# Kernel optimization log

Hardware: AMD Instinct MI355X
Metric: run time of the kernel (lower is better)

Reference implementation:

```python
import jax, jax.numpy as jnp
import numpy as np

NUM_NODES = 100000
IN_CH = 128
OUT_CH = 64
NUM_EDGES = 1000000


def setup_inputs() -> dict:
    key = jax.random.key(0)
    ks = jax.random.split(key, 16)

    x = jax.random.normal(ks[0], (NUM_NODES, IN_CH), dtype=jnp.float32)

    def make_edges(k_src, k_tgt, k_w):
        src = jax.random.randint(k_src, (NUM_EDGES,), 0, NUM_NODES, dtype=jnp.int32)
        # tf.math.segment_sum requires sorted segment ids -> sort targets
        tgt = jnp.sort(jax.random.randint(k_tgt, (NUM_EDGES,), 0, NUM_NODES, dtype=jnp.int32))
        ei = jnp.stack([src, tgt], axis=0)  # (2, E)
        ew = jax.random.uniform(k_w, (NUM_EDGES,), dtype=jnp.float32)
        return ei, ew

    edge_index_in, edge_weight_in = make_edges(ks[1], ks[2], ks[3])
    edge_index_out, edge_weight_out = make_edges(ks[4], ks[5], ks[6])

    glorot = (6.0 / (IN_CH + OUT_CH)) ** 0.5
    W_main_in = jax.random.uniform(ks[7], (IN_CH, OUT_CH), minval=-glorot, maxval=glorot, dtype=jnp.float32)
    W_main_out = jax.random.uniform(ks[8], (IN_CH, OUT_CH), minval=-glorot, maxval=glorot, dtype=jnp.float32)
    W_shared = jax.random.uniform(ks[9], (IN_CH, OUT_CH), minval=-glorot, maxval=glorot, dtype=jnp.float32)

    bias_main_in = jnp.zeros((OUT_CH,), dtype=jnp.float32)
    bias_main_out = jnp.zeros((OUT_CH,), dtype=jnp.float32)
    bias_shared_in = jnp.zeros((OUT_CH,), dtype=jnp.float32)
    bias_shared_out = jnp.zeros((OUT_CH,), dtype=jnp.float32)

    C_in_vec = jnp.ones((NUM_NODES, 1), dtype=jnp.float32)
    C_out_vec = jnp.ones((NUM_NODES, 1), dtype=jnp.float32)

    return {
        "x": x,
        "W_main_in": W_main_in,
        "W_main_out": W_main_out,
        "W_shared": W_shared,
        "bias_main_in": bias_main_in,
        "bias_main_out": bias_main_out,
        "bias_shared_in": bias_shared_in,
        "bias_shared_out": bias_shared_out,
        "C_in_vec": C_in_vec,
        "C_out_vec": C_out_vec,
        "edge_index_in": edge_index_in,
        "edge_weight_in": edge_weight_in,
        "edge_index_out": edge_index_out,
        "edge_weight_out": edge_weight_out,
    }


def _propagate(h, edge_index, edge_weight, num_nodes):
    # gather messages from source nodes, scale by edge weight, sum into targets
    src = edge_index[0]
    tgt = edge_index[1]
    msgs = h[src] * edge_weight[:, None]  # (E, OUT_CH)
    return jax.ops.segment_sum(msgs, tgt, num_segments=num_nodes)  # (N, OUT_CH)


def reference(x, W_main_in, W_main_out, W_shared,
              bias_main_in, bias_main_out, bias_shared_in, bias_shared_out,
              C_in_vec, C_out_vec,
              edge_index_in, edge_weight_in, edge_index_out, edge_weight_out):
    n = x.shape[0]
    h_main_in = _propagate(x @ W_main_in, edge_index_in, edge_weight_in, n)
    h_shared_in = _propagate(x @ W_shared, edge_index_in, edge_weight_in, n)
    ic_combined = h_main_in + bias_main_in + (h_shared_in + bias_shared_in)

    h_main_out = _propagate(x @ W_main_out, edge_index_out, edge_weight_out, n)
    h_shared_out = _propagate(x @ W_shared, edge_index_out, edge_weight_out, n)
    oc_combined = h_main_out + bias_main_out + (h_shared_out + bias_shared_out)

    return C_in_vec * ic_combined + C_out_vec * oc_combined
```

## Files before the change

### kernel.cpp

```cpp
#include <hip/hip_runtime.h>

#define IN_CH   128
#define OUT_CH  64
#define M_TILE  128
#define XS_PITCH 136

typedef __attribute__((ext_vector_type(8))) short short8;
typedef __attribute__((ext_vector_type(4))) float floatx4;

__device__ __forceinline__ unsigned short f2bf(float f) {
    union { float f; unsigned u; } v; v.f = f;
    unsigned r = v.u + 0x7fffu + ((v.u >> 16) & 1u);
    return (unsigned short)(r >> 16);
}
__device__ __forceinline__ float bf2f(unsigned v) {
    union { unsigned u; float f; } c; c.u = v << 16;
    return c.f;
}

__global__ void prep_kernel(const int* __restrict__ tgtIn,
                            const int* __restrict__ tgtOut,
                            const float* __restrict__ Wmi,
                            const float* __restrict__ Wmo,
                            const float* __restrict__ Wsh,
                            int* __restrict__ rpIn,
                            int* __restrict__ rpOut,
                            unsigned short* __restrict__ WcT,
                            int n_nodes, int neIn, int neOut)
{
    int i = blockIdx.x * blockDim.x + threadIdx.x;
    int half = n_nodes + 1;
    if (i < 2 * half) {
        const int* tgt; int* rp; int t; int ne;
        if (i < half) { tgt = tgtIn;  rp = rpIn;  t = i;        ne = neIn; }
        else          { tgt = tgtOut; rp = rpOut; t = i - half; ne = neOut; }
        int lo = 0, hi = ne;
        while (lo < hi) {
            int mid = (lo + hi) >> 1;
            if (tgt[mid] < t) lo = mid + 1; else hi = mid;
        }
        rp[t] = lo;
    } else {
        int j = i - 2 * half;
        if (j < 2 * OUT_CH * IN_CH) {
            int n = j >> 7, k = j & 127;
            float m = (n < OUT_CH) ? Wmi[k * OUT_CH + n]
                                   : Wmo[k * OUT_CH + (n - OUT_CH)];
            float s = Wsh[k * OUT_CH + (n & (OUT_CH - 1))];
            WcT[n * IN_CH + k] = f2bf(m + s);
        }
    }
}

__global__ __launch_bounds__(256, 3)
void gemm_kernel(const float* __restrict__ x,
                 const unsigned short* __restrict__ WcT,
                 unsigned short* __restrict__ Abf,
                 unsigned short* __restrict__ Bbf,
                 int n_nodes)
{
    __shared__ unsigned short Xs[M_TILE][XS_PITCH];

    const int tid  = threadIdx.x;
    const int w    = tid >> 6;
    const int lane = tid & 63;
    const int l15  = lane & 15;
    const int quad = lane >> 4;
    const long long node0 = (long long)blockIdx.x * M_TILE;

    short8 bfrag[4][2];
#pragma unroll
    for (int ks = 0; ks < 4; ++ks)
#pragma unroll
        for (int ni = 0; ni < 2; ++ni)
            bfrag[ks][ni] = *(const short8*)&WcT[(w * 32 + ni * 16 + l15) * IN_CH
                                                 + ks * 32 + quad * 8];

    {
        const float4* x4 = (const float4*)x;
        for (int i = tid; i < M_TILE * (IN_CH / 4); i += 256) {
            int row = i >> 5, c4 = i & 31;
            long long node = node0 + row;
            float4 v = make_float4(0.f, 0.f, 0.f, 0.f);
            if (node < n_nodes) v = x4[node * (IN_CH / 4) + c4];
            uint2 p;
            p.x = ((unsigned)f2bf(v.y) << 16) | f2bf(v.x);
            p.y = ((unsigned)f2bf(v.w) << 16) | f2bf(v.z);
            *(uint2*)&Xs[row][c4 * 4] = p;
        }
    }
    __syncthreads();

    floatx4 acc[8][2];
#pragma unroll
    for (int mi = 0; mi < 8; ++mi)
#pragma unroll
        for (int ni = 0; ni < 2; ++ni)
            acc[mi][ni] = (floatx4){0.f, 0.f, 0.f, 0.f};

#pragma unroll
    for (int ks = 0; ks < 4; ++ks) {
        const int k0 = ks * 32 + quad * 8;
#pragma unroll
        for (int mi = 0; mi < 8; ++mi) {
            short8 a = *(const short8*)&Xs[mi * 16 + l15][k0];
            acc[mi][0] = __builtin_amdgcn_mfma_f32_16x16x32_bf16(a, bfrag[ks][0], acc[mi][0], 0, 0, 0);
            acc[mi][1] = __builtin_amdgcn_mfma_f32_16x16x32_bf16(a, bfrag[ks][1], acc[mi][1], 0, 0, 0);
        }
    }

    unsigned short* Hout = (w < 2) ? Abf : Bbf;
    const int colb = (w & 1) * 32;
#pragma unroll
    for (int mi = 0; mi < 8; ++mi)
#pragma unroll
        for (int ni = 0; ni < 2; ++ni)
#pragma unroll
            for (int r = 0; r < 4; ++r) {
                long long row = node0 + mi * 16 + quad * 4 + r;
                if (row < n_nodes)
                    Hout[row * OUT_CH + colb + ni * 16 + l15] = f2bf(acc[mi][ni][r]);
            }
}

__device__ __forceinline__
float segsum(const unsigned short* __restrict__ Hl, int e0, int e1,
             const int* __restrict__ src, const float* __restrict__ ew,
             int lane)
{
    float a0 = 0.f, a1 = 0.f, a2 = 0.f, a3 = 0.f;
    for (int base = e0; base < e1; base += 64) {
        int cnt = min(64, e1 - base);
        int s = 0; float w = 0.f;
        if (lane < cnt) { s = src[base + lane]; w = ew[base + lane]; }
        for (int j = 0; j < cnt; j += 8) {
            int sj[8]; float wj[8];
#pragma unroll
            for (int i = 0; i < 8; ++i) {
                int idx = j + i;
                int sel = (idx < cnt) ? idx : 0;
                sj[i] = __builtin_amdgcn_readlane(s, sel);
                int wi = __builtin_amdgcn_readlane(__float_as_int(w), sel);
                wj[i] = (idx < cnt) ? __int_as_float(wi) : 0.f;
            }
            float v[8];
#pragma unroll
            for (int i = 0; i < 8; ++i)
                v[i] = bf2f(Hl[(long long)sj[i] * OUT_CH]);
            a0 += wj[0] * v[0]; a1 += wj[1] * v[1];
            a2 += wj[2] * v[2]; a3 += wj[3] * v[3];
            a0 += wj[4] * v[4]; a1 += wj[5] * v[5];
            a2 += wj[6] * v[6]; a3 += wj[7] * v[7];
        }
    }
    return (a0 + a1) + (a2 + a3);
}

__global__ __launch_bounds__(256)
void prop_kernel(const unsigned short* __restrict__ A,
                 const unsigned short* __restrict__ B,
                 const int* __restrict__ rpIn, const int* __restrict__ rpOut,
                 const int* __restrict__ srcIn, const float* __restrict__ ewIn,
                 const int* __restrict__ srcOut, const float* __restrict__ ewOut,
                 const float* __restrict__ bmi, const float* __restrict__ bmo,
                 const float* __restrict__ bsi, const float* __restrict__ bso,
                 const float* __restrict__ Cin, const float* __restrict__ Cout,
                 float* __restrict__ out, int n_nodes)
{
    const int lane = threadIdx.x & 63;
    const int wv = __builtin_amdgcn_readfirstlane(threadIdx.x >> 6);
    const int t = blockIdx.x * 4 + wv;
    if (t >= n_nodes) return;

    float bin  = bmi[lane] + bsi[lane];
    float bout = bmo[lane] + bso[lane];
    float ci = Cin[t], co = Cout[t];

    int ei0 = __builtin_amdgcn_readfirstlane(rpIn[t]);
    int ei1 = __builtin_amdgcn_readfirstlane(rpIn[t + 1]);
    int eo0 = __builtin_amdgcn_readfirstlane(rpOut[t]);
    int eo1 = __builtin_amdgcn_readfirstlane(rpOut[t + 1]);

    float ic = segsum(A + lane, ei0, ei1, srcIn, ewIn, lane);
    float oc = segsum(B + lane, eo0, eo1, srcOut, ewOut, lane);

    out[t * OUT_CH + lane] = ci * (ic + bin) + co * (oc + bout);
}

extern "C" void kernel_launch(void* const* d_in, const int* in_sizes, int n_in,
                              void* d_out, int out_size, void* d_ws, size_t ws_size,
                              hipStream_t stream)
{
    const float* x    = (const float*)d_in[0];
    const float* Wmi  = (const float*)d_in[1];
    const float* Wmo  = (const float*)d_in[2];
    const float* Wsh  = (const float*)d_in[3];
    const float* bmi  = (const float*)d_in[4];
    const float* bmo  = (const float*)d_in[5];
    const float* bsi  = (const float*)d_in[6];
    const float* bso  = (const float*)d_in[7];
    const float* Cin  = (const float*)d_in[8];
    const float* Cout = (const float*)d_in[9];
    const int*   eiIn  = (const int*)d_in[10];
    const float* ewIn  = (const float*)d_in[11];
    const int*   eiOut = (const int*)d_in[12];
    const float* ewOut = (const float*)d_in[13];

    const int n_nodes = in_sizes[0] / IN_CH;
    const int neIn  = in_sizes[11];
    const int neOut = in_sizes[13];

    const int* srcIn  = eiIn;
    const int* tgtIn  = eiIn + neIn;
    const int* srcOut = eiOut;
    const int* tgtOut = eiOut + neOut;

    char* ws = (char*)d_ws;
    size_t NH = (size_t)n_nodes * OUT_CH * sizeof(unsigned short);
    unsigned short* Abf = (unsigned short*)ws;
    unsigned short* Bbf = (unsigned short*)(ws + NH);
    int* rpIn  = (int*)(ws + 2 * NH);
    int* rpOut = rpIn + (n_nodes + 1);
    unsigned short* WcT = (unsigned short*)(rpOut + (n_nodes + 1));

    int prep_threads = 2 * (n_nodes + 1) + 2 * OUT_CH * IN_CH;
    prep_kernel<<<(prep_threads + 255) / 256, 256, 0, stream>>>(
        tgtIn, tgtOut, Wmi, Wmo, Wsh, rpIn, rpOut, WcT, n_nodes, neIn, neOut);

    int gblocks = (n_nodes + M_TILE - 1) / M_TILE;
    gemm_kernel<<<gblocks, 256, 0, stream>>>(x, WcT, Abf, Bbf, n_nodes);

    prop_kernel<<<(n_nodes + 3) / 4, 256, 0, stream>>>(
        Abf, Bbf, rpIn, rpOut, srcIn, ewIn, srcOut, ewOut,
        bmi, bmo, bsi, bso, Cin, Cout, (float*)d_out, n_nodes);
}
```

Baseline: 211.0 us.

## Split in/out propagation across separate wavefronts and simplify edge loop

The propagation kernel now assigns the in-edge and out-edge segment sums for a node to two different wavefronts instead of running both sequentially in one wave. The B result is passed through shared memory to the A wave, which writes the combined output. The edge loop drops the coalesced index load with readlane broadcast and instead loads the per-edge src and weight scalars directly, unrolled by four. The aim is more parallelism and latency hiding per node, at the cost of a block-wide barrier, twice as many blocks, and scalar index loads in place of one vector load per 64 edges.

```diff
diff --git a/kernel.cpp b/kernel.cpp
--- a/kernel.cpp
+++ b/kernel.cpp
@@ -124,34 +124,24 @@
 }
 
 __device__ __forceinline__
-float segsum(const unsigned short* __restrict__ Hl, int e0, int e1,
+float segsum(const unsigned short* __restrict__ H, int e0, int e1,
              const int* __restrict__ src, const float* __restrict__ ew,
              int lane)
 {
     float a0 = 0.f, a1 = 0.f, a2 = 0.f, a3 = 0.f;
-    for (int base = e0; base < e1; base += 64) {
-        int cnt = min(64, e1 - base);
-        int s = 0; float w = 0.f;
-        if (lane < cnt) { s = src[base + lane]; w = ew[base + lane]; }
-        for (int j = 0; j < cnt; j += 8) {
-            int sj[8]; float wj[8];
-#pragma unroll
-            for (int i = 0; i < 8; ++i) {
-                int idx = j + i;
-                int sel = (idx < cnt) ? idx : 0;
-                sj[i] = __builtin_amdgcn_readlane(s, sel);
-                int wi = __builtin_amdgcn_readlane(__float_as_int(w), sel);
-                wj[i] = (idx < cnt) ? __int_as_float(wi) : 0.f;
-            }
-            float v[8];
-#pragma unroll
-            for (int i = 0; i < 8; ++i)
-                v[i] = bf2f(Hl[(long long)sj[i] * OUT_CH]);
-            a0 += wj[0] * v[0]; a1 += wj[1] * v[1];
-            a2 += wj[2] * v[2]; a3 += wj[3] * v[3];
-            a0 += wj[4] * v[4]; a1 += wj[5] * v[5];
-            a2 += wj[6] * v[6]; a3 += wj[7] * v[7];
-        }
+    int e = e0;
+    for (; e + 4 <= e1; e += 4) {
+        int   s0 = src[e + 0], s1 = src[e + 1], s2 = src[e + 2], s3 = src[e + 3];
+        float w0 = ew[e + 0],  w1 = ew[e + 1],  w2 = ew[e + 2],  w3 = ew[e + 3];
+        float v0 = bf2f(H[s0 * OUT_CH + lane]);
+        float v1 = bf2f(H[s1 * OUT_CH + lane]);
+        float v2 = bf2f(H[s2 * OUT_CH + lane]);
+        float v3 = bf2f(H[s3 * OUT_CH + lane]);
+        a0 += w0 * v0; a1 += w1 * v1; a2 += w2 * v2; a3 += w3 * v3;
+    }
+    for (; e < e1; ++e) {
+        float v = bf2f(H[src[e] * OUT_CH + lane]);
+        a0 += ew[e] * v;
     }
     return (a0 + a1) + (a2 + a3);
 }
@@ -167,24 +157,35 @@
                  const float* __restrict__ Cin, const float* __restrict__ Cout,
                  float* __restrict__ out, int n_nodes)
 {
+    __shared__ float xch[2][OUT_CH];
+
     const int lane = threadIdx.x & 63;
-    const int wv = __builtin_amdgcn_readfirstlane(threadIdx.x >> 6);
-    const int t = blockIdx.x * 4 + wv;
-    if (t >= n_nodes) return;
-
-    float bin  = bmi[lane] + bsi[lane];
-    float bout = bmo[lane] + bso[lane];
-    float ci = Cin[t], co = Cout[t];
-
-    int ei0 = __builtin_amdgcn_readfirstlane(rpIn[t]);
-    int ei1 = __builtin_amdgcn_readfirstlane(rpIn[t + 1]);
-    int eo0 = __builtin_amdgcn_readfirstlane(rpOut[t]);
-    int eo1 = __builtin_amdgcn_readfirstlane(rpOut[t + 1]);
-
-    float ic = segsum(A + lane, ei0, ei1, srcIn, ewIn, lane);
-    float oc = segsum(B + lane, eo0, eo1, srcOut, ewOut, lane);
-
-    out[t * OUT_CH + lane] = ci * (ic + bin) + co * (oc + bout);
+    const int wv   = threadIdx.x >> 6;
+    const int slot = wv >> 1;
+    const int isB  = wv & 1;
+    const int t = blockIdx.x * 2 + slot;
+    const bool valid = (t < n_nodes);
+
+    float acc = 0.f;
+    if (valid) {
+        const unsigned short* H = isB ? B : A;
+        const int*   rp  = isB ? rpOut : rpIn;
+        const int*   src = isB ? srcOut : srcIn;
+        const float* ew  = isB ? ewOut : ewIn;
+        int e0 = __builtin_amdgcn_readfirstlane(rp[t]);
+        int e1 = __builtin_amdgcn_readfirstlane(rp[t + 1]);
+        acc = segsum(H, e0, e1, src, ew, lane);
+    }
+
+    if (isB) xch[slot][lane] = acc;
+    __syncthreads();
+
+    if (!isB && valid) {
+        float oc = xch[slot][lane];
+        float bin  = bmi[lane] + bsi[lane];
+        float bout = bmo[lane] + bso[lane];
+        out[t * OUT_CH + lane] = Cin[t] * (acc + bin) + Cout[t] * (oc + bout);
+    }
 }
 
 extern "C" void kernel_launch(void* const* d_in, const int* in_sizes, int n_in,
@@ -230,7 +231,7 @@
     int gblocks = (n_nodes + M_TILE - 1) / M_TILE;
     gemm_kernel<<<gblocks, 256, 0, stream>>>(x, WcT, Abf, Bbf, n_nodes);
 
-    prop_kernel<<<(n_nodes + 3) / 4, 256, 0, stream>>>(
+    prop_kernel<<<(n_nodes + 1) / 2, 256, 0, stream>>>(
         Abf, Bbf, rpIn, rpOut, srcIn, ewIn, srcOut, ewOut,
         bmi, bmo, bsi, bso, Cin, Cout, (float*)d_out, n_nodes);
 }
```

Result: slower. 254.9 us (+20.8%).
